# Performance work log

Hardware: AMD Instinct MI355X
Metric: run time of the kernel (lower is better)

## Reference

```python
import jax
jax.config.update("jax_enable_x64", True)
import jax.numpy as jnp
from jax import lax
import numpy as np

SR, LOWER, UPPER, ORDER = 16000, 500, 7000, 8


def _butter_bandpass_ba(N, lower, upper, sr):
    """Replicates scipy.signal.butter(N, [2*lo/sr, 2*hi/sr], 'bandpass')."""
    Wn = np.array([2.0 * lower / sr, 2.0 * upper / sr])
    fs = 2.0
    warped = 2.0 * fs * np.tan(np.pi * Wn / fs)  # pre-warp for bilinear
    # analog Butterworth lowpass prototype (buttap)
    m = np.arange(-N + 1, N, 2)
    p = -np.exp(1j * np.pi * m / (2 * N))
    k = 1.0
    # lp2bp_zpk
    bw = warped[1] - warped[0]
    wo = np.sqrt(warped[0] * warped[1])
    degree = len(p)  # no finite zeros in prototype
    p_lp = p * bw / 2.0
    p_bp = np.concatenate([p_lp + np.sqrt(p_lp ** 2 - wo ** 2),
                           p_lp - np.sqrt(p_lp ** 2 - wo ** 2)])
    z_bp = np.zeros(degree, dtype=complex)
    k_bp = k * bw ** degree
    # bilinear_zpk (fs=2)
    fs2 = 2.0 * fs
    z_d = (fs2 + z_bp) / (fs2 - z_bp)
    p_d = (fs2 + p_bp) / (fs2 - p_bp)
    z_d = np.append(z_d, -np.ones(len(p_bp) - len(z_bp)))
    k_d = k_bp * np.real(np.prod(fs2 - z_bp) / np.prod(fs2 - p_bp))
    b = np.real(k_d * np.poly(z_d))
    a = np.real(np.poly(p_d))
    return b, a


def _lfilter_zi(b, a):
    """Replicates scipy.signal.lfilter_zi (steady-state of step response)."""
    n = len(a)
    comp = np.zeros((n - 1, n - 1))
    comp[0, :] = -a[1:] / a[0]
    comp[1:, :-1] = np.eye(n - 2)
    IminusA = np.eye(n - 1) - comp.T
    B = b[1:] - a[1:] * b[0]
    return np.linalg.solve(IminusA, B)


def _lfilter(b, a, x, zi):
    """Direct-form II transposed IIR filter. x: [B, L], zi: [B, n-1]."""
    b0, bt, at = b[0], b[1:], a[1:]

    def step(z, xt):  # z: [B, n-1], xt: [B]
        y = b0 * xt + z[:, 0]
        z_shift = jnp.concatenate([z[:, 1:], jnp.zeros_like(z[:, :1])], axis=1)
        z_new = z_shift + xt[:, None] * bt[None, :] - y[:, None] * at[None, :]
        return z_new, y

    _, y = lax.scan(step, zi, x.T)
    return y.T


def _filtfilt(b, a, x):
    """Replicates scipy.signal.filtfilt defaults (padtype='odd', method='pad')."""
    padlen = 3 * max(len(a), len(b))
    # odd extension along time
    left = 2.0 * x[:, :1] - x[:, 1:padlen + 1][:, ::-1]
    right = 2.0 * x[:, -1:] - x[:, -padlen - 1:-1][:, ::-1]
    ext = jnp.concatenate([left, x, right], axis=1)
    zi = jnp.asarray(_lfilter_zi(b, a))[None, :]  # [1, n-1]
    bj, aj = jnp.asarray(b), jnp.asarray(a)
    y = _lfilter(bj, aj, ext, zi * ext[:, :1])          # forward pass
    yr = y[:, ::-1]
    y = _lfilter(bj, aj, yr, zi * yr[:, :1])            # backward pass
    y = y[:, ::-1]
    return y[:, padlen:-padlen]


def setup_inputs() -> dict:
    key = jax.random.key(0)
    audio = jax.random.normal(key, (32, 262144), dtype=jnp.float32)
    return {"audio": audio}


def reference(audio) -> jnp.ndarray:
    b, a = _butter_bandpass_ba(ORDER, LOWER, UPPER, SR)
    y = _filtfilt(b, a, audio.astype(jnp.float64))
    return y.astype(jnp.float32)
```

## Files before the change

kernel.cpp:

```cpp
#include <hip/hip_runtime.h>
#include <cmath>
#include <complex>

#define NB    32
#define LX    262144
#define PAD   51
#define LTOT  (LX + 2 * PAD)
#define CM    16
#define F_PAD 1946
#define LPAD  (LTOT + F_PAD)
#define TILE  (64 * CM)
#define NTILE (LPAD / TILE)
#define WPB   2
#define NP    8
#define LDSR  17
#define WIN   16
#define WREG  1280

struct CoeffsS { float a1[NP], a2[NP], b0[NP], b1[NP], c0; };
struct LvS { float lv[6][NP][4]; };

__global__ void k_init(float4* __restrict__ mt, LvS L) {
    int id = blockIdx.x * 256 + threadIdx.x;
    if (id >= 512) return;
    int t = id >> 3, q = id & 7;
    float m0 = 1.f, m1 = 0.f, m2 = 0.f, m3 = 1.f;
    for (int k = 0; k < 6; k++)
        if ((t >> k) & 1) {
            float a0 = L.lv[k][q][0], a1 = L.lv[k][q][1];
            float a2 = L.lv[k][q][2], a3 = L.lv[k][q][3];
            float n0 = a0 * m0 + a1 * m2, n1 = a0 * m1 + a1 * m3;
            float n2 = a2 * m0 + a3 * m2, n3 = a2 * m1 + a3 * m3;
            m0 = n0; m1 = n1; m2 = n2; m3 = n3;
        }
    mt[id] = make_float4(m0, m1, m2, m3);
}

__device__ __forceinline__ void load_uA(const float* __restrict__ x,
                                        float base, int c, float (&u)[CM]) {
    int t0 = c * CM - F_PAD;
    if (t0 >= PAD && t0 + CM <= PAD + LX) {
        const float* xs = x + (t0 - PAD);
#pragma unroll
        for (int m = 0; m < CM / 4; m++) {
            float4 v = *reinterpret_cast<const float4*>(xs + 4 * m);
            u[4 * m] = v.x - base; u[4 * m + 1] = v.y - base;
            u[4 * m + 2] = v.z - base; u[4 * m + 3] = v.w - base;
        }
    } else {
#pragma unroll
        for (int i = 0; i < CM; i++) {
            int t = t0 + i;
            float uu;
            if (t < 0) uu = 0.f;
            else {
                float e;
                if (t < PAD)            e = 2.0f * x[0] - x[PAD - t];
                else if (t < PAD + LX)  e = x[t - PAD];
                else                    e = 2.0f * x[LX - 1] - x[2 * LX + PAD - 2 - t];
                uu = e - base;
            }
            u[i] = uu;
        }
    }
}

__device__ __forceinline__ void load_uB(const float* __restrict__ yb,
                                        float base, int c, float (&u)[CM]) {
    if (c < 0) {
#pragma unroll
        for (int i = 0; i < CM; i++) u[i] = 0.f;
        return;
    }
    const float* ys = yb + (size_t)c * CM;
#pragma unroll
    for (int m = 0; m < CM / 4; m++) {
        float4 v = *reinterpret_cast<const float4*>(ys + 4 * m);
        u[4 * m] = v.x - base; u[4 * m + 1] = v.y - base;
        u[4 * m + 2] = v.z - base; u[4 * m + 3] = v.w - base;
    }
}

__device__ __forceinline__ void local_states(const float (&u)[CM], const CoeffsS& C,
                                             float (&w1)[NP], float (&w2)[NP]) {
#pragma unroll
    for (int q = 0; q < NP; q++) { w1[q] = 0.f; w2[q] = 0.f; }
#pragma unroll
    for (int i = 0; i < CM; i++) {
        float uu = u[i];
#pragma unroll
        for (int q = 0; q < NP; q++) {
            float wt = fmaf(C.a1[q], w1[q], fmaf(C.a2[q], w2[q], uu));
            w2[q] = w1[q]; w1[q] = wt;
        }
    }
}

__device__ __forceinline__ void pack_states(float4* sc4, int j,
                                            const float (&w1)[NP], const float (&w2)[NP]) {
#pragma unroll
    for (int p = 0; p < 4; p++)
        sc4[p * 80 + j] = make_float4(w1[2 * p], w2[2 * p], w1[2 * p + 1], w2[2 * p + 1]);
}

template <int PASS>
__global__ __launch_bounds__(128) void k_full(const float* __restrict__ in,
                                              float* __restrict__ outp,
                                              const float4* __restrict__ mt,
                                              CoeffsS C) {
    __shared__ __align__(16) float lds[WPB * WREG];
    int tid = threadIdx.x, wv = tid >> 6, l = tid & 63;
    int ttx = blockIdx.x * WPB + wv, b = blockIdx.y;
    int c = ttx * 64 + l;
    float* wlds = lds + wv * WREG;
    float4* sc4 = reinterpret_cast<float4*>(wlds);

    const float* x = in + (size_t)b * (PASS == 0 ? LX : LPAD);
    float base = (PASS == 0) ? (2.0f * x[0] - x[PAD]) : x[0];

    if (l < WIN) {
        float uw[CM];
        int cw = ttx * 64 - WIN + l;
        if (PASS == 0) load_uA(x, base, cw, uw);
        else           load_uB(x, base, cw, uw);
        float w1[NP], w2[NP];
        local_states(uw, C, w1, w2);
        pack_states(sc4, l, w1, w2);
    }

    float u[CM];
    if (PASS == 0) load_uA(x, base, c, u);
    else           load_uB(x, base, c, u);
    float w1[NP], w2[NP];
    local_states(u, C, w1, w2);
    pack_states(sc4, WIN + l, w1, w2);
    __syncthreads();

    float e1[NP], e2[NP];
#pragma unroll
    for (int q = 0; q < NP; q++) { e1[q] = 0.f; e2[q] = 0.f; }
#pragma unroll
    for (int k = 1; k <= WIN; k++) {
#pragma unroll
        for (int p = 0; p < 4; p++) {
            float4 f = sc4[p * 80 + WIN + l - k];
            float4 ma = mt[(k - 1) * NP + 2 * p];
            float4 mb = mt[(k - 1) * NP + 2 * p + 1];
            e1[2 * p]     = fmaf(ma.x, f.x, fmaf(ma.y, f.y, e1[2 * p]));
            e2[2 * p]     = fmaf(ma.z, f.x, fmaf(ma.w, f.y, e2[2 * p]));
            e1[2 * p + 1] = fmaf(mb.x, f.z, fmaf(mb.y, f.w, e1[2 * p + 1]));
            e2[2 * p + 1] = fmaf(mb.z, f.z, fmaf(mb.w, f.w, e2[2 * p + 1]));
        }
    }

#pragma unroll
    for (int q = 0; q < NP; q++) { w1[q] = e1[q]; w2[q] = e2[q]; }
#pragma unroll
    for (int i = 0; i < CM; i++) {
        float uu = u[i];
        float y = C.c0 * uu;
#pragma unroll
        for (int q = 0; q < NP; q++) {
            float wt = fmaf(C.a1[q], w1[q], fmaf(C.a2[q], w2[q], uu));
            y = fmaf(C.b0[q], wt, fmaf(C.b1[q], w1[q], y));
            w2[q] = w1[q]; w1[q] = wt;
        }
        u[i] = y;
    }

    __syncthreads();
#pragma unroll
    for (int i = 0; i < CM; i++) wlds[l * LDSR + i] = u[i];
    __syncthreads();

    if (PASS == 0) {
        float4* yb4 = reinterpret_cast<float4*>(
            outp + (size_t)b * LPAD + (size_t)(NTILE - 1 - ttx) * TILE);
#pragma unroll
        for (int k = 0; k < 4; k++) {
            int o4 = l + 64 * k;
            int ts = 63 - (o4 >> 2);
            int ih = 15 - 4 * (o4 & 3);
            const float* r = &wlds[ts * LDSR];
            yb4[o4] = make_float4(r[ih], r[ih - 1], r[ih - 2], r[ih - 3]);
        }
    } else {
        float* ob = outp + (size_t)b * LX;
        int J0 = (LTOT - 1 - PAD) - ttx * TILE;
#pragma unroll
        for (int it = 0; it < CM; it++) {
            int o = it * 64 + l;
            int j = J0 - o;
            if (j >= 0 && j < LX)
                ob[j] = wlds[(o >> 4) * LDSR + (o & 15)];
        }
    }
}

static void compute_coeffs(CoeffsS& C, LvS& L) {
    using cd = std::complex<double>;
    const int N = 8;
    const double sr = 16000.0, lo = 500.0, hi = 7000.0, fs = 2.0;
    double w0 = 2.0 * fs * std::tan(M_PI * (2.0 * lo / sr) / fs);
    double w1 = 2.0 * fs * std::tan(M_PI * (2.0 * hi / sr) / fs);
    double bw = w1 - w0, wo = std::sqrt(w0 * w1);
    cd pbp[16];
    for (int k = 0; k < N; k++) {
        int m = -N + 1 + 2 * k;
        cd pl = -std::exp(cd(0.0, M_PI * m / (2.0 * N)));
        pl *= bw / 2.0;
        cd s = std::sqrt(pl * pl - cd(wo * wo, 0.0));
        pbp[k] = pl + s; pbp[k + N] = pl - s;
    }
    double kbp = std::pow(bw, (double)N);
    const double fs2 = 4.0;
    cd pd[16], denom = 1.0;
    for (int i = 0; i < 16; i++) {
        pd[i] = (cd(fs2, 0.0) + pbp[i]) / (cd(fs2, 0.0) - pbp[i]);
        denom *= (cd(fs2, 0.0) - pbp[i]);
    }
    double kd = kbp * std::real(cd(std::pow(fs2, 8.0), 0.0) / denom);
    cd prodp = 1.0;
    for (int i = 0; i < 16; i++) prodp *= pd[i];
    cd c0 = cd(kd, 0.0) / prodp;
    int n = 0;
    for (int i = 0; i < 16; i++) {
        if (pd[i].imag() <= 0.0) continue;
        cd inv = 1.0 / pd[i];
        cd t1 = cd(1.0, 0.0) - inv, t2 = cd(1.0, 0.0) + inv;
        cd numr = cd(kd, 0.0);
        for (int k = 0; k < 8; k++) numr *= t1;
        for (int k = 0; k < 8; k++) numr *= t2;
        cd den = 1.0;
        for (int j = 0; j < 16; j++)
            if (j != i) den *= (cd(1.0, 0.0) - pd[j] * inv);
        cd r2 = 2.0 * numr / den;
        if (n < NP) {
            double a1 = 2.0 * pd[i].real();
            double a2 = -std::norm(pd[i]);
            C.a1[n] = (float)a1; C.a2[n] = (float)a2;
            C.b0[n] = (float)r2.real();
            C.b1[n] = (float)(-(r2.real() * pd[i].real() + r2.imag() * pd[i].imag()));
            double M[4] = { a1, a2, 1.0, 0.0 };
            for (int s = 0; s < 4; s++) {
                double q0 = M[0] * M[0] + M[1] * M[2], q1 = M[0] * M[1] + M[1] * M[3];
                double q2 = M[2] * M[0] + M[3] * M[2], q3 = M[2] * M[1] + M[3] * M[3];
                M[0] = q0; M[1] = q1; M[2] = q2; M[3] = q3;
            }
            for (int k = 0; k < 6; k++) {
                for (int j = 0; j < 4; j++) L.lv[k][n][j] = (float)M[j];
                double q0 = M[0] * M[0] + M[1] * M[2], q1 = M[0] * M[1] + M[1] * M[3];
                double q2 = M[2] * M[0] + M[3] * M[2], q3 = M[2] * M[1] + M[3] * M[3];
                M[0] = q0; M[1] = q1; M[2] = q2; M[3] = q3;
            }
            n++;
        }
    }
    C.c0 = (float)c0.real();
}

extern "C" void kernel_launch(void* const* d_in, const int* in_sizes, int n_in,
                              void* d_out, int out_size, void* d_ws, size_t ws_size,
                              hipStream_t stream) {
    const float* audio = (const float*)d_in[0];
    float* out = (float*)d_out;

    CoeffsS C; LvS L;
    compute_coeffs(C, L);

    char* ws = (char*)d_ws;
    size_t o = 0;
    auto alloc = [&](size_t bytes) { size_t r = o; o += (bytes + 255) & ~(size_t)255; return r; };
    float*  ybuf = (float*)(ws + alloc((size_t)NB * LPAD * sizeof(float)));
    float4* mt   = (float4*)(ws + alloc(512 * sizeof(float4)));

    dim3 blk(128), g(NTILE / WPB, NB);

    k_init   <<<2, 256, 0, stream>>>(mt, L);
    k_full<0><<<g, blk, 0, stream>>>(audio, ybuf, mt, C);
    k_full<1><<<g, blk, 0, stream>>>(ybuf, out, mt, C);
}
```

Before: 66.71 us.

## Fuse forward and backward filter passes into one tiled kernel with halo recompute

Replaces the two-kernel scheme, where the forward pass wrote a reversed intermediate buffer to global memory and a second kernel ran the backward pass, with one fused kernel. Each 1024-sample tile recomputes forward outputs over an overlapping halo, keeps them in shared memory, and runs the backward pass with windowed state combination. The goal is to cut the intermediate global round trip and one kernel launch. The cost is extra halo recompute, which relies on the filter states decaying within the window, plus smaller 64-thread blocks.

```diff
diff --git a/kernel.cpp b/kernel.cpp
--- a/kernel.cpp
+++ b/kernel.cpp
@@ -7,25 +7,22 @@
 #define PAD   51
 #define LTOT  (LX + 2 * PAD)
 #define CM    16
-#define F_PAD 1946
-#define LPAD  (LTOT + F_PAD)
-#define TILE  (64 * CM)
-#define NTILE (LPAD / TILE)
-#define WPB   2
+#define NTX   256
 #define NP    8
-#define LDSR  17
 #define WIN   16
-#define WREG  1280
+#define NRELY 80
+#define SCS   100
+#define YLDSR 17
 
 struct CoeffsS { float a1[NP], a2[NP], b0[NP], b1[NP], c0; };
-struct LvS { float lv[6][NP][4]; };
+struct LvS { float lv[4][NP][4]; };
 
 __global__ void k_init(float4* __restrict__ mt, LvS L) {
-    int id = blockIdx.x * 256 + threadIdx.x;
-    if (id >= 512) return;
+    int id = threadIdx.x;
+    if (id >= 128) return;
     int t = id >> 3, q = id & 7;
     float m0 = 1.f, m1 = 0.f, m2 = 0.f, m3 = 1.f;
-    for (int k = 0; k < 6; k++)
+    for (int k = 0; k < 4; k++)
         if ((t >> k) & 1) {
             float a0 = L.lv[k][q][0], a1 = L.lv[k][q][1];
             float a2 = L.lv[k][q][2], a3 = L.lv[k][q][3];
@@ -36,9 +33,8 @@
     mt[id] = make_float4(m0, m1, m2, m3);
 }
 
-__device__ __forceinline__ void load_uA(const float* __restrict__ x,
-                                        float base, int c, float (&u)[CM]) {
-    int t0 = c * CM - F_PAD;
+__device__ __forceinline__ void load_u(const float* __restrict__ x, float base,
+                                       int t0, float (&u)[CM]) {
     if (t0 >= PAD && t0 + CM <= PAD + LX) {
         const float* xs = x + (t0 - PAD);
 #pragma unroll
@@ -52,7 +48,7 @@
         for (int i = 0; i < CM; i++) {
             int t = t0 + i;
             float uu;
-            if (t < 0) uu = 0.f;
+            if (t < 0 || t >= LTOT) uu = 0.f;
             else {
                 float e;
                 if (t < PAD)            e = 2.0f * x[0] - x[PAD - t];
@@ -65,24 +61,8 @@
     }
 }
 
-__device__ __forceinline__ void load_uB(const float* __restrict__ yb,
-                                        float base, int c, float (&u)[CM]) {
-    if (c < 0) {
-#pragma unroll
-        for (int i = 0; i < CM; i++) u[i] = 0.f;
-        return;
-    }
-    const float* ys = yb + (size_t)c * CM;
-#pragma unroll
-    for (int m = 0; m < CM / 4; m++) {
-        float4 v = *reinterpret_cast<const float4*>(ys + 4 * m);
-        u[4 * m] = v.x - base; u[4 * m + 1] = v.y - base;
-        u[4 * m + 2] = v.z - base; u[4 * m + 3] = v.w - base;
-    }
-}
-
-__device__ __forceinline__ void local_states(const float (&u)[CM], const CoeffsS& C,
-                                             float (&w1)[NP], float (&w2)[NP]) {
+__device__ __forceinline__ void states_fwd(const float (&u)[CM], const CoeffsS& C,
+                                           float (&w1)[NP], float (&w2)[NP]) {
 #pragma unroll
     for (int q = 0; q < NP; q++) { w1[q] = 0.f; w2[q] = 0.f; }
 #pragma unroll
@@ -96,54 +76,25 @@
     }
 }
 
-__device__ __forceinline__ void pack_states(float4* sc4, int j,
+__device__ __forceinline__ void pack_states(float4* sc4, int rel,
                                             const float (&w1)[NP], const float (&w2)[NP]) {
 #pragma unroll
     for (int p = 0; p < 4; p++)
-        sc4[p * 80 + j] = make_float4(w1[2 * p], w2[2 * p], w1[2 * p + 1], w2[2 * p + 1]);
-}
-
-template <int PASS>
-__global__ __launch_bounds__(128) void k_full(const float* __restrict__ in,
-                                              float* __restrict__ outp,
-                                              const float4* __restrict__ mt,
-                                              CoeffsS C) {
-    __shared__ __align__(16) float lds[WPB * WREG];
-    int tid = threadIdx.x, wv = tid >> 6, l = tid & 63;
-    int ttx = blockIdx.x * WPB + wv, b = blockIdx.y;
-    int c = ttx * 64 + l;
-    float* wlds = lds + wv * WREG;
-    float4* sc4 = reinterpret_cast<float4*>(wlds);
-
-    const float* x = in + (size_t)b * (PASS == 0 ? LX : LPAD);
-    float base = (PASS == 0) ? (2.0f * x[0] - x[PAD]) : x[0];
-
-    if (l < WIN) {
-        float uw[CM];
-        int cw = ttx * 64 - WIN + l;
-        if (PASS == 0) load_uA(x, base, cw, uw);
-        else           load_uB(x, base, cw, uw);
-        float w1[NP], w2[NP];
-        local_states(uw, C, w1, w2);
-        pack_states(sc4, l, w1, w2);
-    }
-
-    float u[CM];
-    if (PASS == 0) load_uA(x, base, c, u);
-    else           load_uB(x, base, c, u);
-    float w1[NP], w2[NP];
-    local_states(u, C, w1, w2);
-    pack_states(sc4, WIN + l, w1, w2);
-    __syncthreads();
-
-    float e1[NP], e2[NP];
+        sc4[p * SCS + rel] = make_float4(w1[2 * p], w2[2 * p], w1[2 * p + 1], w2[2 * p + 1]);
+}
+
+template <int DIR>
+__device__ __forceinline__ void combine_win(const float4* sc4,
+                                            const float4* __restrict__ mt, int rel,
+                                            float (&e1)[NP], float (&e2)[NP]) {
 #pragma unroll
     for (int q = 0; q < NP; q++) { e1[q] = 0.f; e2[q] = 0.f; }
 #pragma unroll
     for (int k = 1; k <= WIN; k++) {
+        int rr = rel + DIR * k;
 #pragma unroll
         for (int p = 0; p < 4; p++) {
-            float4 f = sc4[p * 80 + WIN + l - k];
+            float4 f = sc4[p * SCS + rr];
             float4 ma = mt[(k - 1) * NP + 2 * p];
             float4 mb = mt[(k - 1) * NP + 2 * p + 1];
             e1[2 * p]     = fmaf(ma.x, f.x, fmaf(ma.y, f.y, e1[2 * p]));
@@ -152,7 +103,12 @@
             e2[2 * p + 1] = fmaf(mb.z, f.z, fmaf(mb.w, f.w, e2[2 * p + 1]));
         }
     }
-
+}
+
+__device__ __forceinline__ void replay_fwd(const float (&u)[CM], const CoeffsS& C,
+                                           const float (&e1)[NP], const float (&e2)[NP],
+                                           float* __restrict__ yrow) {
+    float w1[NP], w2[NP];
 #pragma unroll
     for (int q = 0; q < NP; q++) { w1[q] = e1[q]; w2[q] = e2[q]; }
 #pragma unroll
@@ -165,35 +121,109 @@
             y = fmaf(C.b0[q], wt, fmaf(C.b1[q], w1[q], y));
             w2[q] = w1[q]; w1[q] = wt;
         }
-        u[i] = y;
-    }
-
+        yrow[i] = y;
+    }
+}
+
+__device__ __forceinline__ void bstate_store(const float* __restrict__ yrow, int rel,
+                                             int TS, float bc, const CoeffsS& C,
+                                             float4* sc4) {
+    float w1[NP], w2[NP];
+#pragma unroll
+    for (int q = 0; q < NP; q++) { w1[q] = 0.f; w2[q] = 0.f; }
+#pragma unroll
+    for (int i = CM - 1; i >= 0; --i) {
+        float v = yrow[i] - bc;
+        if (TS + 16 * rel + i >= LTOT) v = 0.f;
+#pragma unroll
+        for (int q = 0; q < NP; q++) {
+            float wt = fmaf(C.a1[q], w1[q], fmaf(C.a2[q], w2[q], v));
+            w2[q] = w1[q]; w1[q] = wt;
+        }
+    }
+    pack_states(sc4, rel, w1, w2);
+}
+
+__global__ __launch_bounds__(64) void k_fused(const float* __restrict__ in,
+                                              float* __restrict__ outp,
+                                              const float4* __restrict__ mt,
+                                              CoeffsS C) {
+    __shared__ __align__(16) float4 sc4[4 * SCS];
+    __shared__ float ylds[NRELY * YLDSR];
+    int l = threadIdx.x, tx = blockIdx.x, b = blockIdx.y;
+    const float* x = in + (size_t)b * LX;
+    float base = 2.0f * x[0] - x[PAD];
+    int TS = 1024 * tx - 205;
+    bool lastT = (tx == NTX - 1);
+
+    float uA[CM];
+    load_u(x, base, TS + 16 * (16 + l), uA);
+    {
+        float w1[NP], w2[NP];
+        states_fwd(uA, C, w1, w2);
+        pack_states(sc4, 16 + l, w1, w2);
+    }
+    int relB = (l < 16) ? l : ((l < 32) ? 64 + l : -1);
+    if (relB >= 0) {
+        float uB[CM];
+        load_u(x, base, TS + 16 * relB, uB);
+        float w1[NP], w2[NP];
+        states_fwd(uB, C, w1, w2);
+        pack_states(sc4, relB, w1, w2);
+    }
     __syncthreads();
-#pragma unroll
-    for (int i = 0; i < CM; i++) wlds[l * LDSR + i] = u[i];
+
+    {
+        int rel = 16 + l;
+        float e1[NP], e2[NP];
+        combine_win<-1>(sc4, mt, rel, e1, e2);
+        replay_fwd(uA, C, e1, e2, &ylds[(rel - 16) * YLDSR]);
+    }
+    if (l < 16) {
+        int rel = 80 + l;
+        float uB[CM];
+        load_u(x, base, TS + 16 * rel, uB);
+        float e1[NP], e2[NP];
+        combine_win<-1>(sc4, mt, rel, e1, e2);
+        replay_fwd(uB, C, e1, e2, &ylds[(rel - 16) * YLDSR]);
+    }
     __syncthreads();
 
-    if (PASS == 0) {
-        float4* yb4 = reinterpret_cast<float4*>(
-            outp + (size_t)b * LPAD + (size_t)(NTILE - 1 - ttx) * TILE);
-#pragma unroll
-        for (int k = 0; k < 4; k++) {
-            int o4 = l + 64 * k;
-            int ts = 63 - (o4 >> 2);
-            int ih = 15 - 4 * (o4 & 3);
-            const float* r = &wlds[ts * LDSR];
-            yb4[o4] = make_float4(r[ih], r[ih - 1], r[ih - 2], r[ih - 3]);
-        }
-    } else {
-        float* ob = outp + (size_t)b * LX;
-        int J0 = (LTOT - 1 - PAD) - ttx * TILE;
-#pragma unroll
-        for (int it = 0; it < CM; it++) {
-            int o = it * 64 + l;
-            int j = J0 - o;
-            if (j >= 0 && j < LX)
-                ob[j] = wlds[(o >> 4) * LDSR + (o & 15)];
-        }
+    float bc = lastT ? ylds[67 * YLDSR + 2] : 0.f;
+
+    bstate_store(&ylds[(17 + l - 16) * YLDSR], 17 + l, TS, bc, C, sc4);
+    if (l < 15)
+        bstate_store(&ylds[(81 + l - 16) * YLDSR], 81 + l, TS, bc, C, sc4);
+    __syncthreads();
+
+    {
+        int relZ = 16 + l;
+        float e1[NP], e2[NP];
+        combine_win<+1>(sc4, mt, relZ, e1, e2);
+        float* yr = &ylds[l * YLDSR];
+        float w1[NP], w2[NP];
+#pragma unroll
+        for (int q = 0; q < NP; q++) { w1[q] = e1[q]; w2[q] = e2[q]; }
+#pragma unroll
+        for (int i = CM - 1; i >= 0; --i) {
+            float v = yr[i] - bc;
+            float z = C.c0 * v;
+#pragma unroll
+            for (int q = 0; q < NP; q++) {
+                float wt = fmaf(C.a1[q], w1[q], fmaf(C.a2[q], w2[q], v));
+                z = fmaf(C.b0[q], wt, fmaf(C.b1[q], w1[q], z));
+                w2[q] = w1[q]; w1[q] = wt;
+            }
+            yr[i] = z;
+        }
+    }
+    __syncthreads();
+
+    float* ob = outp + (size_t)b * LX + (size_t)tx * 1024;
+#pragma unroll
+    for (int it = 0; it < CM; it++) {
+        int o = it * 64 + l;
+        ob[o] = ylds[(o >> 4) * YLDSR + (o & 15)];
     }
 }
 
@@ -247,7 +277,7 @@
                 double q2 = M[2] * M[0] + M[3] * M[2], q3 = M[2] * M[1] + M[3] * M[3];
                 M[0] = q0; M[1] = q1; M[2] = q2; M[3] = q3;
             }
-            for (int k = 0; k < 6; k++) {
+            for (int k = 0; k < 4; k++) {
                 for (int j = 0; j < 4; j++) L.lv[k][n][j] = (float)M[j];
                 double q0 = M[0] * M[0] + M[1] * M[2], q1 = M[0] * M[1] + M[1] * M[3];
                 double q2 = M[2] * M[0] + M[3] * M[2], q3 = M[2] * M[1] + M[3] * M[3];
@@ -268,15 +298,10 @@
     CoeffsS C; LvS L;
     compute_coeffs(C, L);
 
-    char* ws = (char*)d_ws;
-    size_t o = 0;
-    auto alloc = [&](size_t bytes) { size_t r = o; o += (bytes + 255) & ~(size_t)255; return r; };
-    float*  ybuf = (float*)(ws + alloc((size_t)NB * LPAD * sizeof(float)));
-    float4* mt   = (float4*)(ws + alloc(512 * sizeof(float4)));
-
-    dim3 blk(128), g(NTILE / WPB, NB);
-
-    k_init   <<<2, 256, 0, stream>>>(mt, L);
-    k_full<0><<<g, blk, 0, stream>>>(audio, ybuf, mt, C);
-    k_full<1><<<g, blk, 0, stream>>>(ybuf, out, mt, C);
-}
+    float4* mt = (float4*)d_ws;
+
+    dim3 g(NTX, NB), blkw(64);
+
+    k_init <<<1, 128, 0, stream>>>(mt, L);
+    k_fused<<<g, blkw, 0, stream>>>(audio, out, mt, C);
+}
```

Measured after the change: 89.37 us. 34.0% more time.
